# Optimization experiments

Hardware: AMD Instinct MI355X
Metric: run time of the kernel (lower is better)

The kernel has to match this reference:

```python
import jax, jax.numpy as jnp
import numpy as np

N_QUBITS = 12
N_LAYERS = 5
DIM = 2 ** N_QUBITS
B = 4096


def _rz(a):
    # Rz(a) = diag(e^{-ia/2}, e^{ia/2})
    z = jnp.zeros((), jnp.complex64)
    em = jnp.exp(-0.5j * a.astype(jnp.complex64))
    ep = jnp.exp(0.5j * a.astype(jnp.complex64))
    return jnp.stack([jnp.stack([em, z]), jnp.stack([z, ep])])


def _ry(a):
    c = jnp.cos(0.5 * a).astype(jnp.complex64)
    s = jnp.sin(0.5 * a).astype(jnp.complex64)
    return jnp.stack([jnp.stack([c, -s]), jnp.stack([s, c])])


def _apply_1q(state, U, q):
    # shared 2x2 gate U on qubit q (qubit 0 = MSB); state (B, 2^n)
    bsz = state.shape[0]
    st = state.reshape(bsz, 2 ** q, 2, -1)
    st = jnp.einsum('st,blsr->bltr', U, st)
    return st.reshape(bsz, -1)


def _apply_1q_batched(state, U, q):
    # per-sample gates U (B,2,2) on qubit q
    bsz = state.shape[0]
    st = state.reshape(bsz, 2 ** q, 2, -1)
    st = jnp.einsum('bst,blsr->bltr', U, st)
    return st.reshape(bsz, -1)


def _apply_cnot(state, q):
    # control q, target q+1 (adjacent); flip target slice where control=1
    bsz = state.shape[0]
    st = state.reshape(bsz, 2 ** q, 2, 2, -1)
    st = jnp.stack([st[:, :, 0], jnp.flip(st[:, :, 1], axis=2)], axis=2)
    return st.reshape(bsz, -1)


def _qnn_states(X, params):
    # X: (B, n_qubits) float, params: (n_layers, n_qubits, 3) float
    bsz = X.shape[0]
    state = jnp.zeros((bsz, DIM), jnp.complex64).at[:, 0].set(1.0)
    for l in range(N_LAYERS):
        for q in range(N_QUBITS):
            phi, theta, lam = params[l, q, 0], params[l, q, 1], params[l, q, 2]
            # circuit applies Rz(phi), then Ry(theta), then Rz(lam)
            U = _rz(lam) @ _ry(theta) @ _rz(phi)
            state = _apply_1q(state, U, q)
            if l == N_LAYERS - 1:
                a = X[:, q]
                c = jnp.cos(0.5 * a).astype(jnp.complex64)
                s = jnp.sin(0.5 * a).astype(jnp.complex64)
                G = jnp.stack([jnp.stack([c, -s], -1), jnp.stack([s, c], -1)], -2)  # (B,2,2)
                state = _apply_1q_batched(state, G, q)
        # CNOT chain entanglement
        for q in range(N_QUBITS - 1):
            state = _apply_cnot(state, q)
    return state


def setup_inputs() -> dict:
    key = jax.random.key(0)
    k1, k2 = jax.random.split(key)
    X = jax.random.uniform(k1, (B, N_QUBITS), dtype=jnp.float32) * (2.0 * np.pi)
    params = jax.random.normal(k2, (N_LAYERS, N_QUBITS, 3), dtype=jnp.float32) * 0.01
    return {"X": X, "params": params}


def reference(X, params):
    states = _qnn_states(X, params)  # (B, 2^n) complex64
    # Neural EQK (n-to-n): K[i,j] = |<psi_i | psi_j>|^2
    G = states @ states.conj().T  # (B, B) complex
    K = jnp.real(G * jnp.conj(G)).astype(jnp.float32)
    return K
```

## Files before the change

kernel.cpp:

```cpp
#include <hip/hip_runtime.h>
#include <hip/hip_bf16.h>

#define NQ 12
#define NL 5
#define DIM 4096
#define BATCH 4096
#define TILE 128
#define BK 64
#define NIT (DIM / BK)
#define NTILE (BATCH / TILE)
#define NBLK (NTILE * (NTILE + 1) / 2)
#define NXCD 8
#define CPX (NBLK / NXCD)

typedef __bf16 bf16x8 __attribute__((ext_vector_type(8)));
typedef float f32x16 __attribute__((ext_vector_type(16)));
typedef unsigned int u32x4 __attribute__((ext_vector_type(4)));
typedef unsigned short u16x8 __attribute__((ext_vector_type(8)));
typedef unsigned int u32;
typedef unsigned short u16;

#define MFMA32(a, b, c) __builtin_amdgcn_mfma_f32_32x32x16_bf16(a, b, c, 0, 0, 0)

__device__ static inline u16 f32_to_bf16_bits(float x) {
    u32 b = __builtin_bit_cast(u32, x);
    b += 0x7fffu + ((b >> 16) & 1u);
    return (u16)(b >> 16);
}

__device__ static inline void async_copy16(const void* g, void* l) {
    __builtin_amdgcn_global_load_lds((const __attribute__((address_space(1))) u32*)g,
                                     (__attribute__((address_space(3))) u32*)l, 16, 0, 0);
}

__device__ static inline float2 cmul(float2 m, float2 a) {
    return make_float2(m.x * a.x - m.y * a.y, m.x * a.y + m.y * a.x);
}
__device__ static inline float2 cadd(float2 a, float2 b) {
    return make_float2(a.x + b.x, a.y + b.y);
}

__device__ static inline void tile_of(int p, int* bi, int* bj) {
    int rem = p, b = 0;
    while (rem >= NTILE - b) { rem -= NTILE - b; ++b; }
    *bi = b; *bj = b + rem;
}

__global__ __launch_bounds__(1024) void qnn_base(const float* __restrict__ params,
                                                 float2* __restrict__ psi1) {
    __shared__ float2 st[DIM];
    __shared__ float2 U[NL * NQ][4];
    const int t = threadIdx.x;

    for (int k = t; k < DIM; k += 1024) st[k] = make_float2(k == 0 ? 1.f : 0.f, 0.f);

    if (t < NL * NQ) {
        float phi = params[t * 3 + 0], th = params[t * 3 + 1], lam = params[t * 3 + 2];
        float c = cosf(0.5f * th), s = sinf(0.5f * th);
        float ap = 0.5f * (lam + phi), am = 0.5f * (lam - phi);
        U[t][0] = make_float2(c * cosf(ap), -c * sinf(ap));
        U[t][1] = make_float2(s * cosf(am), s * sinf(am));
        U[t][2] = make_float2(-s * cosf(am), s * sinf(am));
        U[t][3] = make_float2(c * cosf(ap), c * sinf(ap));
    }
    __syncthreads();

    for (int l = 0; l < NL; ++l) {
        for (int qq = 0; qq < NQ; qq += 2) {
            const float2* M1 = U[l * NQ + qq];
            const float2* M2 = U[l * NQ + qq + 1];
            const int b2 = 10 - qq;
            const int s2 = 1 << b2, s1 = s2 << 1;
            int hi = t >> b2, lo = t & (s2 - 1);
            int i00 = (hi << (b2 + 2)) | lo;
            int i01 = i00 + s2, i10 = i00 + s1, i11 = i10 + s2;
            float2 a00 = st[i00], a01 = st[i01], a10 = st[i10], a11 = st[i11];
            float2 b00 = cadd(cmul(M1[0], a00), cmul(M1[1], a10));
            float2 b10 = cadd(cmul(M1[2], a00), cmul(M1[3], a10));
            float2 b01 = cadd(cmul(M1[0], a01), cmul(M1[1], a11));
            float2 b11 = cadd(cmul(M1[2], a01), cmul(M1[3], a11));
            st[i00] = cadd(cmul(M2[0], b00), cmul(M2[1], b01));
            st[i01] = cadd(cmul(M2[2], b00), cmul(M2[3], b01));
            st[i10] = cadd(cmul(M2[0], b10), cmul(M2[1], b11));
            st[i11] = cadd(cmul(M2[2], b10), cmul(M2[3], b11));
            __syncthreads();
        }
        if (l < NL - 1) {
            float2 v[4];
            #pragma unroll
            for (int u = 0; u < 4; ++u) {
                int k = t * 4 + u, j = k;
                #pragma unroll
                for (int q = 10; q >= 0; --q) j ^= ((j >> (11 - q)) & 1) << (10 - q);
                v[u] = st[j];
            }
            __syncthreads();
            #pragma unroll
            for (int u = 0; u < 4; ++u) st[t * 4 + u] = v[u];
            __syncthreads();
        }
    }
    for (int k = t; k < DIM; k += 1024) psi1[k] = st[k];
}

__global__ __launch_bounds__(256) void qnn_m(const float2* __restrict__ psi1,
                                             float2* __restrict__ m) {
    __shared__ float2 st[DIM];
    __shared__ float2 red[4];
    const int t = threadIdx.x;
    for (int k = t; k < DIM; k += 256) st[k] = psi1[k];
    __syncthreads();
    for (int xi = 0; xi < 16; ++xi) {
        const int x = blockIdx.x * 16 + xi;
        float sre = 0.f, sim = 0.f;
        for (int d = t; d < DIM; d += 256) {
            float2 a = st[d];
            float2 b = st[d ^ x];
            float sgn = (__popc(x & ~d) & 1) ? -1.f : 1.f;
            sre += sgn * (a.x * b.x + a.y * b.y);
            sim += sgn * (a.y * b.x - a.x * b.y);
        }
        #pragma unroll
        for (int o = 32; o; o >>= 1) {
            sre += __shfl_down(sre, o);
            sim += __shfl_down(sim, o);
        }
        if ((t & 63) == 0) red[t >> 6] = make_float2(sre, sim);
        __syncthreads();
        if (t == 0)
            m[x] = make_float2(red[0].x + red[1].x + red[2].x + red[3].x,
                               red[0].y + red[1].y + red[2].y + red[3].y);
        __syncthreads();
    }
}

__global__ __launch_bounds__(1024) void qnn_wu(const float* __restrict__ X,
                                               const float2* __restrict__ m,
                                               u16* __restrict__ WR,
                                               u16* __restrict__ WI) {
    __shared__ float2 st[DIM];
    __shared__ float cs[NQ], sn[NQ];
    const int b = blockIdx.x;
    const int t = threadIdx.x;

    for (int k = t; k < DIM; k += 1024) st[k] = m[k];
    if (t < NQ) {
        float a = 0.5f * X[b * NQ + t];
        cs[t] = cosf(a); sn[t] = sinf(a);
    }
    __syncthreads();

    for (int qq = 0; qq < NQ; qq += 2) {
        const float c1 = cs[qq], s1v = sn[qq];
        const float c2 = cs[qq + 1], s2v = sn[qq + 1];
        const int b2 = 10 - qq;
        const int s2 = 1 << b2, s1 = s2 << 1;
        int hi = t >> b2, lo = t & (s2 - 1);
        int i00 = (hi << (b2 + 2)) | lo;
        int i01 = i00 + s2, i10 = i00 + s1, i11 = i10 + s2;
        float2 a00 = st[i00], a01 = st[i01], a10 = st[i10], a11 = st[i11];
        float2 b00 = make_float2(c1 * a00.x + s1v * a10.x, c1 * a00.y + s1v * a10.y);
        float2 b10 = make_float2(s1v * a00.x - c1 * a10.x, s1v * a00.y - c1 * a10.y);
        float2 b01 = make_float2(c1 * a01.x + s1v * a11.x, c1 * a01.y + s1v * a11.y);
        float2 b11 = make_float2(s1v * a01.x - c1 * a11.x, s1v * a01.y - c1 * a11.y);
        st[i00] = make_float2(c2 * b00.x + s2v * b01.x, c2 * b00.y + s2v * b01.y);
        st[i01] = make_float2(s2v * b00.x - c2 * b01.x, s2v * b00.y - c2 * b01.y);
        st[i10] = make_float2(c2 * b10.x + s2v * b11.x, c2 * b10.y + s2v * b11.y);
        st[i11] = make_float2(s2v * b10.x - c2 * b11.x, s2v * b10.y - c2 * b11.y);
        __syncthreads();
    }

    u16 hr[4], hi4[4];
    #pragma unroll
    for (int u = 0; u < 4; ++u) {
        float2 a = st[t * 4 + u];
        hr[u] = f32_to_bf16_bits(a.x);
        hi4[u] = f32_to_bf16_bits(a.y);
    }
    *(ushort4*)&WR[(size_t)b * DIM + t * 4] = make_ushort4(hr[0], hr[1], hr[2], hr[3]);
    *(ushort4*)&WI[(size_t)b * DIM + t * 4] = make_ushort4(hi4[0], hi4[1], hi4[2], hi4[3]);
}

__global__ __launch_bounds__(256, 2) void qnn_gram2(const u16* __restrict__ WR,
                                                    const u16* __restrict__ WI,
                                                    const float* __restrict__ X,
                                                    float* __restrict__ K) {
    const int p = (blockIdx.x % NXCD) * CPX + blockIdx.x / NXCD;
    int bi, bj;
    tile_of(p, &bi, &bj);

    __shared__ __align__(16) unsigned char lds[4][TILE][64];
    const int t = threadIdx.x;
    const int w = t >> 6, lane = t & 63;
    const int half = lane >> 5, l31 = lane & 31;
    const int wm = (w >> 1) * 64, wn = (w & 1) * 64;
    const int rowA = bi * TILE, rowB = bj * TILE;
    const int srow16 = lane >> 2;
    const int sphys = lane & 3;

    f32x16 accRe[2][2], accIm[2][2];
    #pragma unroll
    for (int a = 0; a < 2; ++a)
        #pragma unroll
        for (int b = 0; b < 2; ++b) {
            #pragma unroll
            for (int r = 0; r < 16; ++r) { accRe[a][b][r] = 0.f; accIm[a][b][r] = 0.f; }
        }

    float csh[2][6], snh[2][6], Umid[2][4], Ud[2][8];
    #pragma unroll
    for (int ni = 0; ni < 2; ++ni) {
        const int j = rowB + wn + ni * 32 + l31;
        float c[NQ], s[NQ];
        #pragma unroll
        for (int q = 0; q < NQ; ++q) {
            float a = 0.5f * X[j * NQ + q];
            c[q] = cosf(a); s[q] = sinf(a);
        }
        #pragma unroll
        for (int q = 0; q < 6; ++q) { csh[ni][q] = c[q]; snh[ni][q] = s[q]; }
        #pragma unroll
        for (int k16 = 0; k16 < 4; ++k16) {
            float f6 = (k16 & 2) ? s[6] : c[6];
            float f7 = (k16 & 1) ? s[7] : c[7];
            float f8 = half ? s[8] : c[8];
            Umid[ni][k16] = f6 * f7 * f8;
        }
        #pragma unroll
        for (int d = 0; d < 8; ++d)
            Ud[ni][d] = ((d & 4) ? s[9] : c[9]) * ((d & 2) ? s[10] : c[10])
                      * ((d & 1) ? s[11] : c[11]);
    }

#define ISSUE2(it)                                                                      \
    do {                                                                                \
        const size_t kbase = (size_t)(it) * (BK * 2);                                   \
        _Pragma("unroll")                                                               \
        for (int pl = 0; pl < 2; ++pl) {                                                \
            const u16* src = pl ? WI : WR;                                              \
            _Pragma("unroll")                                                           \
            for (int kh = 0; kh < 2; ++kh) {                                            \
                _Pragma("unroll")                                                       \
                for (int jj = 0; jj < 2; ++jj) {                                        \
                    int s = w * 2 + jj;                                                 \
                    int row = s * 16 + srow16;                                          \
                    int logc = sphys ^ ((row >> 1) & 3);                                \
                    const char* gp = (const char*)src                                   \
                        + (size_t)(rowA + row) * (DIM * 2) + kbase + kh * 64            \
                        + logc * 16;                                                    \
                    char* lp = (char*)lds + (pl * 2 + kh) * 8192 + s * 1024;            \
                    async_copy16(gp, lp);                                               \
                }                                                                       \
            }                                                                           \
        }                                                                               \
    } while (0)

    ISSUE2(0);
    for (int it = 0; it < NIT; ++it) {
        __syncthreads();

        bf16x8 fWR[2][4], fWI[2][4];
        #pragma unroll
        for (int mi = 0; mi < 2; ++mi) {
            int r = wm + mi * 32 + l31;
            int sw = (r >> 1) & 3;
            #pragma unroll
            for (int k16 = 0; k16 < 4; ++k16) {
                int kh = k16 >> 1;
                int phys = (((k16 & 1) * 2 + half) ^ sw);
                fWR[mi][k16] = *(const bf16x8*)((const char*)lds + (0 + kh) * 8192 + r * 64 + phys * 16);
                fWI[mi][k16] = *(const bf16x8*)((const char*)lds + (2 + kh) * 8192 + r * 64 + phys * 16);
            }
        }

        __syncthreads();
        if (it + 1 < NIT) ISSUE2(it + 1);

        float Uhi[2];
        #pragma unroll
        for (int ni = 0; ni < 2; ++ni) {
            float v = ((it >> 5) & 1) ? snh[ni][0] : csh[ni][0];
            v *= ((it >> 4) & 1) ? snh[ni][1] : csh[ni][1];
            v *= ((it >> 3) & 1) ? snh[ni][2] : csh[ni][2];
            v *= ((it >> 2) & 1) ? snh[ni][3] : csh[ni][3];
            v *= ((it >> 1) & 1) ? snh[ni][4] : csh[ni][4];
            v *= (it & 1) ? snh[ni][5] : csh[ni][5];
            Uhi[ni] = v;
        }
        bf16x8 fU[2][4];
        #pragma unroll
        for (int ni = 0; ni < 2; ++ni)
            #pragma unroll
            for (int k16 = 0; k16 < 4; ++k16) {
                float sc = Uhi[ni] * Umid[ni][k16];
                u16x8 h;
                #pragma unroll
                for (int d = 0; d < 8; ++d)
                    h[d] = f32_to_bf16_bits(sc * Ud[ni][d]);
                fU[ni][k16] = __builtin_bit_cast(bf16x8, h);
            }

        #pragma unroll
        for (int k16 = 0; k16 < 4; ++k16) {
            #pragma unroll
            for (int mi = 0; mi < 2; ++mi)
                #pragma unroll
                for (int ni = 0; ni < 2; ++ni)
                    accRe[mi][ni] = MFMA32(fWR[mi][k16], fU[ni][k16], accRe[mi][ni]);
            #pragma unroll
            for (int mi = 0; mi < 2; ++mi)
                #pragma unroll
                for (int ni = 0; ni < 2; ++ni)
                    accIm[mi][ni] = MFMA32(fWI[mi][k16], fU[ni][k16], accIm[mi][ni]);
        }
    }
#undef ISSUE2

    const int iBase = rowA + wm;
    const int jBase = rowB + wn;
    #pragma unroll
    for (int mi = 0; mi < 2; ++mi)
        #pragma unroll
        for (int ni = 0; ni < 2; ++ni)
            #pragma unroll
            for (int r = 0; r < 16; ++r) {
                int row32 = (r & 3) + 8 * (r >> 2) + 4 * half;
                int i = iBase + mi * 32 + row32;
                int j = jBase + ni * 32 + l31;
                float re = accRe[mi][ni][r];
                float im = accIm[mi][ni][r];
                float v = re * re + im * im;
                if (i == j) v = 1.0f;
                K[(size_t)i * BATCH + j] = v;
                if (bi != bj) K[(size_t)j * BATCH + i] = v;
            }
}

extern "C" void kernel_launch(void* const* d_in, const int* in_sizes, int n_in,
                              void* d_out, int out_size, void* d_ws, size_t ws_size,
                              hipStream_t stream) {
    const float* X = (const float*)d_in[0];
    const float* params = (const float*)d_in[1];
    float* K = (float*)d_out;

    const size_t plane = (size_t)BATCH * DIM * sizeof(u16);
    float2* psi1 = (float2*)d_ws;
    float2* m = (float2*)((char*)d_ws + 65536);
    u16* WR = (u16*)((char*)d_ws + 131072);
    u16* WI = (u16*)((char*)WR + plane);

    hipLaunchKernelGGL(qnn_base, dim3(1), dim3(1024), 0, stream, params, psi1);
    hipLaunchKernelGGL(qnn_m, dim3(256), dim3(256), 0, stream, psi1, m);
    hipLaunchKernelGGL(qnn_wu, dim3(BATCH), dim3(1024), 0, stream, X, m, WR, WI);
    hipLaunchKernelGGL(qnn_gram2, dim3(NBLK), dim3(256), 0, stream, WR, WI, X, K);
}
```

Measured before the change: 429.5 us.

## Retile gram kernel to 64x256 tiles and pack bf16 conversion

Changes the symmetric gram kernel from 128x128 triangular tiles to 64-row by 256-column tiles over the lower triangle (544 blocks). Each wave now covers a 64-column slice and all 64 rows, so the LDS staging of the W operand is halved. The U operand is generated per k16 step using the packed v_cvt_pk_bf16_f32 instruction instead of manual rounding. Diagonal-crossing tiles now mirror writes per element (i != j), which can write some entries twice. The new tiling trades loading less of W per block for more blocks and more redundant on-the-fly U generation.

New measurement: 390.8 us. 1.1x faster.

```diff
diff --git a/kernel.cpp b/kernel.cpp
--- a/kernel.cpp
+++ b/kernel.cpp
@@ -5,18 +5,19 @@
 #define NL 5
 #define DIM 4096
 #define BATCH 4096
-#define TILE 128
 #define BK 64
 #define NIT (DIM / BK)
-#define NTILE (BATCH / TILE)
-#define NBLK (NTILE * (NTILE + 1) / 2)
+#define TROW 64
+#define TCOL 256
+#define NRT (BATCH / TROW)
+#define NCT (BATCH / TCOL)
+#define NBLK3 544
 #define NXCD 8
-#define CPX (NBLK / NXCD)
+#define CPX3 (NBLK3 / NXCD)
 
 typedef __bf16 bf16x8 __attribute__((ext_vector_type(8)));
 typedef float f32x16 __attribute__((ext_vector_type(16)));
 typedef unsigned int u32x4 __attribute__((ext_vector_type(4)));
-typedef unsigned short u16x8 __attribute__((ext_vector_type(8)));
 typedef unsigned int u32;
 typedef unsigned short u16;
 
@@ -28,6 +29,12 @@
     return (u16)(b >> 16);
 }
 
+__device__ static inline u32 cvt_pk_bf16(float lo, float hi) {
+    u32 r;
+    asm volatile("v_cvt_pk_bf16_f32 %0, %1, %2" : "=v"(r) : "v"(lo), "v"(hi));
+    return r;
+}
+
 __device__ static inline void async_copy16(const void* g, void* l) {
     __builtin_amdgcn_global_load_lds((const __attribute__((address_space(1))) u32*)g,
                                      (__attribute__((address_space(3))) u32*)l, 16, 0, 0);
@@ -40,10 +47,10 @@
     return make_float2(a.x + b.x, a.y + b.y);
 }
 
-__device__ static inline void tile_of(int p, int* bi, int* bj) {
-    int rem = p, b = 0;
-    while (rem >= NTILE - b) { rem -= NTILE - b; ++b; }
-    *bi = b; *bj = b + rem;
+__device__ static inline void tile3_of(int p, int* rt, int* ct) {
+    int c = 0, rem = p;
+    while (rem >= 4 * c + 4) { rem -= 4 * c + 4; ++c; }
+    *ct = c; *rt = rem;
 }
 
 __global__ __launch_bounds__(1024) void qnn_base(const float* __restrict__ params,
@@ -181,20 +188,20 @@
     *(ushort4*)&WI[(size_t)b * DIM + t * 4] = make_ushort4(hi4[0], hi4[1], hi4[2], hi4[3]);
 }
 
-__global__ __launch_bounds__(256, 2) void qnn_gram2(const u16* __restrict__ WR,
+__global__ __launch_bounds__(256, 2) void qnn_gram3(const u16* __restrict__ WR,
                                                     const u16* __restrict__ WI,
                                                     const float* __restrict__ X,
                                                     float* __restrict__ K) {
-    const int p = (blockIdx.x % NXCD) * CPX + blockIdx.x / NXCD;
-    int bi, bj;
-    tile_of(p, &bi, &bj);
-
-    __shared__ __align__(16) unsigned char lds[4][TILE][64];
+    const int p = (blockIdx.x % NXCD) * CPX3 + blockIdx.x / NXCD;
+    int rt, ct;
+    tile3_of(p, &rt, &ct);
+
+    __shared__ __align__(16) unsigned char lds[4][TROW][64];
     const int t = threadIdx.x;
     const int w = t >> 6, lane = t & 63;
     const int half = lane >> 5, l31 = lane & 31;
-    const int wm = (w >> 1) * 64, wn = (w & 1) * 64;
-    const int rowA = bi * TILE, rowB = bj * TILE;
+    const int wn = w * 64;
+    const int rowA = rt * TROW, colB = ct * TCOL;
     const int srow16 = lane >> 2;
     const int sphys = lane & 3;
 
@@ -210,7 +217,7 @@
     float csh[2][6], snh[2][6], Umid[2][4], Ud[2][8];
     #pragma unroll
     for (int ni = 0; ni < 2; ++ni) {
-        const int j = rowB + wn + ni * 32 + l31;
+        const int j = colB + wn + ni * 32 + l31;
         float c[NQ], s[NQ];
         #pragma unroll
         for (int q = 0; q < NQ; ++q) {
@@ -232,7 +239,7 @@
                       * ((d & 1) ? s[11] : c[11]);
     }
 
-#define ISSUE2(it)                                                                      \
+#define ISSUE3(it)                                                                      \
     do {                                                                                \
         const size_t kbase = (size_t)(it) * (BK * 2);                                   \
         _Pragma("unroll")                                                               \
@@ -240,41 +247,37 @@
             const u16* src = pl ? WI : WR;                                              \
             _Pragma("unroll")                                                           \
             for (int kh = 0; kh < 2; ++kh) {                                            \
-                _Pragma("unroll")                                                       \
-                for (int jj = 0; jj < 2; ++jj) {                                        \
-                    int s = w * 2 + jj;                                                 \
-                    int row = s * 16 + srow16;                                          \
-                    int logc = sphys ^ ((row >> 1) & 3);                                \
-                    const char* gp = (const char*)src                                   \
-                        + (size_t)(rowA + row) * (DIM * 2) + kbase + kh * 64            \
-                        + logc * 16;                                                    \
-                    char* lp = (char*)lds + (pl * 2 + kh) * 8192 + s * 1024;            \
-                    async_copy16(gp, lp);                                               \
-                }                                                                       \
+                int row = w * 16 + srow16;                                              \
+                int logc = sphys ^ ((row >> 1) & 3);                                    \
+                const char* gp = (const char*)src                                       \
+                    + (size_t)(rowA + row) * (DIM * 2) + kbase + kh * 64                \
+                    + logc * 16;                                                        \
+                char* lp = (char*)lds + (pl * 2 + kh) * 4096 + w * 1024;                \
+                async_copy16(gp, lp);                                                   \
             }                                                                           \
         }                                                                               \
     } while (0)
 
-    ISSUE2(0);
+    ISSUE3(0);
     for (int it = 0; it < NIT; ++it) {
         __syncthreads();
 
         bf16x8 fWR[2][4], fWI[2][4];
         #pragma unroll
         for (int mi = 0; mi < 2; ++mi) {
-            int r = wm + mi * 32 + l31;
+            int r = mi * 32 + l31;
             int sw = (r >> 1) & 3;
             #pragma unroll
             for (int k16 = 0; k16 < 4; ++k16) {
                 int kh = k16 >> 1;
                 int phys = (((k16 & 1) * 2 + half) ^ sw);
-                fWR[mi][k16] = *(const bf16x8*)((const char*)lds + (0 + kh) * 8192 + r * 64 + phys * 16);
-                fWI[mi][k16] = *(const bf16x8*)((const char*)lds + (2 + kh) * 8192 + r * 64 + phys * 16);
+                fWR[mi][k16] = *(const bf16x8*)((const char*)lds + (0 + kh) * 4096 + r * 64 + phys * 16);
+                fWI[mi][k16] = *(const bf16x8*)((const char*)lds + (2 + kh) * 4096 + r * 64 + phys * 16);
             }
         }
 
         __syncthreads();
-        if (it + 1 < NIT) ISSUE2(it + 1);
+        if (it + 1 < NIT) ISSUE3(it + 1);
 
         float Uhi[2];
         #pragma unroll
@@ -287,37 +290,34 @@
             v *= (it & 1) ? snh[ni][5] : csh[ni][5];
             Uhi[ni] = v;
         }
-        bf16x8 fU[2][4];
-        #pragma unroll
-        for (int ni = 0; ni < 2; ++ni)
-            #pragma unroll
-            for (int k16 = 0; k16 < 4; ++k16) {
+
+        #pragma unroll
+        for (int k16 = 0; k16 < 4; ++k16) {
+            bf16x8 fU[2];
+            #pragma unroll
+            for (int ni = 0; ni < 2; ++ni) {
                 float sc = Uhi[ni] * Umid[ni][k16];
-                u16x8 h;
-                #pragma unroll
-                for (int d = 0; d < 8; ++d)
-                    h[d] = f32_to_bf16_bits(sc * Ud[ni][d]);
-                fU[ni][k16] = __builtin_bit_cast(bf16x8, h);
+                u32x4 h;
+                h[0] = cvt_pk_bf16(sc * Ud[ni][0], sc * Ud[ni][1]);
+                h[1] = cvt_pk_bf16(sc * Ud[ni][2], sc * Ud[ni][3]);
+                h[2] = cvt_pk_bf16(sc * Ud[ni][4], sc * Ud[ni][5]);
+                h[3] = cvt_pk_bf16(sc * Ud[ni][6], sc * Ud[ni][7]);
+                fU[ni] = __builtin_bit_cast(bf16x8, h);
             }
-
-        #pragma unroll
-        for (int k16 = 0; k16 < 4; ++k16) {
             #pragma unroll
             for (int mi = 0; mi < 2; ++mi)
                 #pragma unroll
                 for (int ni = 0; ni < 2; ++ni)
-                    accRe[mi][ni] = MFMA32(fWR[mi][k16], fU[ni][k16], accRe[mi][ni]);
+                    accRe[mi][ni] = MFMA32(fWR[mi][k16], fU[ni], accRe[mi][ni]);
             #pragma unroll
             for (int mi = 0; mi < 2; ++mi)
                 #pragma unroll
                 for (int ni = 0; ni < 2; ++ni)
-                    accIm[mi][ni] = MFMA32(fWI[mi][k16], fU[ni][k16], accIm[mi][ni]);
-        }
-    }
-#undef ISSUE2
-
-    const int iBase = rowA + wm;
-    const int jBase = rowB + wn;
+                    accIm[mi][ni] = MFMA32(fWI[mi][k16], fU[ni], accIm[mi][ni]);
+        }
+    }
+#undef ISSUE3
+
     #pragma unroll
     for (int mi = 0; mi < 2; ++mi)
         #pragma unroll
@@ -325,14 +325,14 @@
             #pragma unroll
             for (int r = 0; r < 16; ++r) {
                 int row32 = (r & 3) + 8 * (r >> 2) + 4 * half;
-                int i = iBase + mi * 32 + row32;
-                int j = jBase + ni * 32 + l31;
+                int i = rowA + mi * 32 + row32;
+                int j = colB + wn + ni * 32 + l31;
                 float re = accRe[mi][ni][r];
                 float im = accIm[mi][ni][r];
                 float v = re * re + im * im;
                 if (i == j) v = 1.0f;
                 K[(size_t)i * BATCH + j] = v;
-                if (bi != bj) K[(size_t)j * BATCH + i] = v;
+                if (i != j) K[(size_t)j * BATCH + i] = v;
             }
 }
 
@@ -352,5 +352,5 @@
     hipLaunchKernelGGL(qnn_base, dim3(1), dim3(1024), 0, stream, params, psi1);
     hipLaunchKernelGGL(qnn_m, dim3(256), dim3(256), 0, stream, psi1, m);
     hipLaunchKernelGGL(qnn_wu, dim3(BATCH), dim3(1024), 0, stream, X, m, WR, WI);
-    hipLaunchKernelGGL(qnn_gram2, dim3(NBLK), dim3(256), 0, stream, WR, WI, X, K);
-}
+    hipLaunchKernelGGL(qnn_gram3, dim3(NBLK3), dim3(256), 0, stream, WR, WI, X, K);
+}
```
